# Kernel optimization log

Hardware: AMD Instinct MI355X
Metric: run time of the kernel (lower is better)

Reference implementation:

```python
import jax, jax.numpy as jnp
import numpy as np

def setup_inputs() -> dict:
    key = jax.random.key(0)
    k1, k2 = jax.random.split(key)
    bb_feats = jax.random.normal(k1, (8, 512, 128, 128), dtype=jnp.float32)
    aux_out = jax.random.normal(k2, (8, 19, 128, 128), dtype=jnp.float32)
    return {"bb_feats": bb_feats, "aux_out": aux_out}

def reference(bb_feats, aux_out):
    B, K, H, W = aux_out.shape
    C = bb_feats.shape[1]
    probs = jax.nn.softmax(aux_out.reshape(B, K, H * W), axis=2)  # [B,K,HW]
    feats = bb_feats.reshape(B, C, H * W)                          # [B,C,HW]
    # weighted sum over spatial dim: [B,K,HW] x [B,C,HW] -> [B,K,C]
    ctx = jnp.einsum('bks,bcs->bkc', probs, feats)
    # -> [B,C,K,1]
    return jnp.transpose(ctx, (0, 2, 1))[..., None]
```

## Files before the change

kernel.cpp:

```cpp
#include <hip/hip_runtime.h>
#include <math.h>

#define B 8
#define C 512
#define K 19
#define HW 16384
#define L2E 1.44269504088896340736f

#define CPW 8
#define SCHUNK 4096
#define NSC (HW / SCHUNK)
#define CPB (CPW * 4)
#define CG (C / CPB)

__global__ __launch_bounds__(256)
void softmax_stats_kernel(const float* __restrict__ aux, float* __restrict__ stats) {
    int row = blockIdx.x;
    const float4* x4 = (const float4*)(aux + (size_t)row * HW);
    int tid = threadIdx.x;

    float m = -INFINITY;
    for (int i = tid; i < HW / 4; i += 256) {
        float4 v = x4[i];
        m = fmaxf(m, fmaxf(fmaxf(v.x, v.y), fmaxf(v.z, v.w)));
    }
    #pragma unroll
    for (int off = 32; off > 0; off >>= 1) m = fmaxf(m, __shfl_xor(m, off, 64));
    __shared__ float red[4];
    if ((tid & 63) == 0) red[tid >> 6] = m;
    __syncthreads();
    m = fmaxf(fmaxf(red[0], red[1]), fmaxf(red[2], red[3]));
    __syncthreads();

    float ssum = 0.f;
    for (int i = tid; i < HW / 4; i += 256) {
        float4 v = x4[i];
        ssum += exp2f((v.x - m) * L2E);
        ssum += exp2f((v.y - m) * L2E);
        ssum += exp2f((v.z - m) * L2E);
        ssum += exp2f((v.w - m) * L2E);
    }
    #pragma unroll
    for (int off = 32; off > 0; off >>= 1) ssum += __shfl_xor(ssum, off, 64);
    if ((tid & 63) == 0) red[tid >> 6] = ssum;
    __syncthreads();
    if (tid == 0) {
        float Z = red[0] + red[1] + red[2] + red[3];
        stats[row * 2]     = -m * L2E;
        stats[row * 2 + 1] = 1.0f / Z;
    }
}

__global__ __launch_bounds__(256, 2)
void gather_kernel(const float* __restrict__ feats, const float* __restrict__ aux,
                   const float* __restrict__ stats, float* __restrict__ out) {
    int bid  = blockIdx.x;
    int sc   = bid & (NSC - 1);
    int cg   = (bid / NSC) & (CG - 1);
    int b    = bid / (NSC * CG);
    int lane = threadIdx.x & 63;
    int wave = threadIdx.x >> 6;
    int c0   = cg * CPB + wave * CPW;

    const float* Abase = aux   + (size_t)b * K * HW;
    const float* Fbase = feats + ((size_t)b * C + c0) * HW;
    const float* S     = stats + (size_t)b * K * 2;

    float negml[K], invz[K];
    #pragma unroll
    for (int k = 0; k < K; k++) { negml[k] = S[2 * k]; invz[k] = S[2 * k + 1]; }

    float acc[CPW][K];
    #pragma unroll
    for (int c = 0; c < CPW; c++)
        #pragma unroll
        for (int k = 0; k < K; k++) acc[c][k] = 0.f;

    int s0 = sc * SCHUNK + lane;
    for (int step = 0; step < SCHUNK / 64; step++) {
        int s = s0 + step * 64;
        float p[K];
        #pragma unroll
        for (int k = 0; k < K; k++) {
            float a = Abase[(size_t)k * HW + s];
            p[k] = exp2f(fmaf(a, L2E, negml[k])) * invz[k];
        }
        #pragma unroll
        for (int c = 0; c < CPW; c++) {
            float f = Fbase[(size_t)c * HW + s];
            #pragma unroll
            for (int k = 0; k < K; k++) acc[c][k] = fmaf(p[k], f, acc[c][k]);
        }
    }

    #pragma unroll
    for (int c = 0; c < CPW; c++)
        #pragma unroll
        for (int k = 0; k < K; k++) {
            float v = acc[c][k];
            #pragma unroll
            for (int off = 32; off > 0; off >>= 1) v += __shfl_xor(v, off, 64);
            acc[c][k] = v;
        }

    if (lane == 0) {
        #pragma unroll
        for (int c = 0; c < CPW; c++)
            #pragma unroll
            for (int k = 0; k < K; k++)
                atomicAdd(&out[((size_t)b * C + c0 + c) * K + k], acc[c][k]);
    }
}

extern "C" void kernel_launch(void* const* d_in, const int* in_sizes, int n_in,
                              void* d_out, int out_size, void* d_ws, size_t ws_size,
                              hipStream_t stream) {
    const float* feats = (const float*)d_in[0];
    const float* aux   = (const float*)d_in[1];
    float* out   = (float*)d_out;
    float* stats = (float*)d_ws;

    hipMemsetAsync(d_out, 0, (size_t)out_size * sizeof(float), stream);
    softmax_stats_kernel<<<B * K, 256, 0, stream>>>(aux, stats);
    gather_kernel<<<B * CG * NSC, 256, 0, stream>>>(feats, aux, stats, out);
}
```

Baseline: 482.7 us.

## Share softmax probabilities across waves via LDS and vectorize feature loads

After: 1.368 ms. +183.4%, slower.

```diff
diff --git a/kernel.cpp b/kernel.cpp
--- a/kernel.cpp
+++ b/kernel.cpp
@@ -7,34 +7,42 @@
 #define HW 16384
 #define L2E 1.44269504088896340736f
 
-#define CPW 8
-#define SCHUNK 4096
-#define NSC (HW / SCHUNK)
-#define CPB (CPW * 4)
+#define NW 4
+#define CPW 4
+#define CPB (CPW * NW)
 #define CG (C / CPB)
+#define NSC 4
+#define SCHUNK (HW / NSC)
+#define TS 256
+#define NT (SCHUNK / TS)
 
-__global__ __launch_bounds__(256)
+__global__ __launch_bounds__(1024)
 void softmax_stats_kernel(const float* __restrict__ aux, float* __restrict__ stats) {
     int row = blockIdx.x;
     const float4* x4 = (const float4*)(aux + (size_t)row * HW);
-    int tid = threadIdx.x;
+    int tid  = threadIdx.x;
+    int lane = tid & 63;
+    int wave = tid >> 6;
+    __shared__ float red[16];
 
     float m = -INFINITY;
-    for (int i = tid; i < HW / 4; i += 256) {
-        float4 v = x4[i];
+    #pragma unroll
+    for (int i = 0; i < 4; i++) {
+        float4 v = x4[tid + i * 1024];
         m = fmaxf(m, fmaxf(fmaxf(v.x, v.y), fmaxf(v.z, v.w)));
     }
     #pragma unroll
     for (int off = 32; off > 0; off >>= 1) m = fmaxf(m, __shfl_xor(m, off, 64));
-    __shared__ float red[4];
-    if ((tid & 63) == 0) red[tid >> 6] = m;
+    if (lane == 0) red[wave] = m;
     __syncthreads();
-    m = fmaxf(fmaxf(red[0], red[1]), fmaxf(red[2], red[3]));
+    #pragma unroll
+    for (int w = 0; w < 16; w++) m = fmaxf(m, red[w]);
     __syncthreads();
 
     float ssum = 0.f;
-    for (int i = tid; i < HW / 4; i += 256) {
-        float4 v = x4[i];
+    #pragma unroll
+    for (int i = 0; i < 4; i++) {
+        float4 v = x4[tid + i * 1024];
         ssum += exp2f((v.x - m) * L2E);
         ssum += exp2f((v.y - m) * L2E);
         ssum += exp2f((v.z - m) * L2E);
@@ -42,33 +50,41 @@
     }
     #pragma unroll
     for (int off = 32; off > 0; off >>= 1) ssum += __shfl_xor(ssum, off, 64);
-    if ((tid & 63) == 0) red[tid >> 6] = ssum;
+    if (lane == 0) red[wave] = ssum;
     __syncthreads();
     if (tid == 0) {
-        float Z = red[0] + red[1] + red[2] + red[3];
+        float Z = 0.f;
+        #pragma unroll
+        for (int w = 0; w < 16; w++) Z += red[w];
         stats[row * 2]     = -m * L2E;
         stats[row * 2 + 1] = 1.0f / Z;
     }
 }
 
-__global__ __launch_bounds__(256, 2)
+__global__ __launch_bounds__(256, 4)
 void gather_kernel(const float* __restrict__ feats, const float* __restrict__ aux,
                    const float* __restrict__ stats, float* __restrict__ out) {
+    __shared__ float plds[K][TS];
+
     int bid  = blockIdx.x;
     int sc   = bid & (NSC - 1);
     int cg   = (bid / NSC) & (CG - 1);
     int b    = bid / (NSC * CG);
-    int lane = threadIdx.x & 63;
-    int wave = threadIdx.x >> 6;
+    int tid  = threadIdx.x;
+    int lane = tid & 63;
+    int wave = tid >> 6;
     int c0   = cg * CPB + wave * CPW;
 
-    const float* Abase = aux   + (size_t)b * K * HW;
-    const float* Fbase = feats + ((size_t)b * C + c0) * HW;
+    const float* Abase = aux   + (size_t)b * K * HW + sc * SCHUNK;
+    const float* Fbase = feats + ((size_t)b * C + c0) * HW + sc * SCHUNK;
     const float* S     = stats + (size_t)b * K * 2;
 
     float negml[K], invz[K];
     #pragma unroll
-    for (int k = 0; k < K; k++) { negml[k] = S[2 * k]; invz[k] = S[2 * k + 1]; }
+    for (int k = 0; k < K; k++) {
+        negml[k] = __int_as_float(__builtin_amdgcn_readfirstlane(__float_as_int(S[2 * k])));
+        invz[k]  = __int_as_float(__builtin_amdgcn_readfirstlane(__float_as_int(S[2 * k + 1])));
+    }
 
     float acc[CPW][K];
     #pragma unroll
@@ -76,20 +92,31 @@
         #pragma unroll
         for (int k = 0; k < K; k++) acc[c][k] = 0.f;
 
-    int s0 = sc * SCHUNK + lane;
-    for (int step = 0; step < SCHUNK / 64; step++) {
-        int s = s0 + step * 64;
-        float p[K];
+    for (int t = 0; t < NT; t++) {
+        int s0 = t * TS;
+
+        __syncthreads();
         #pragma unroll
         for (int k = 0; k < K; k++) {
-            float a = Abase[(size_t)k * HW + s];
-            p[k] = exp2f(fmaf(a, L2E, negml[k])) * invz[k];
+            float a = Abase[k * HW + s0 + tid];
+            plds[k][tid] = exp2f(fmaf(a, L2E, negml[k])) * invz[k];
         }
+        __syncthreads();
+
+        float4 f[CPW];
         #pragma unroll
-        for (int c = 0; c < CPW; c++) {
-            float f = Fbase[(size_t)c * HW + s];
+        for (int c = 0; c < CPW; c++)
+            f[c] = *(const float4*)(Fbase + c * HW + s0 + lane * 4);
+        #pragma unroll
+        for (int k = 0; k < K; k++) {
+            float4 p4 = *(const float4*)(&plds[k][lane * 4]);
             #pragma unroll
-            for (int k = 0; k < K; k++) acc[c][k] = fmaf(p[k], f, acc[c][k]);
+            for (int c = 0; c < CPW; c++) {
+                acc[c][k] = fmaf(p4.x, f[c].x, acc[c][k]);
+                acc[c][k] = fmaf(p4.y, f[c].y, acc[c][k]);
+                acc[c][k] = fmaf(p4.z, f[c].z, acc[c][k]);
+                acc[c][k] = fmaf(p4.w, f[c].w, acc[c][k]);
+            }
         }
     }
 
@@ -100,16 +127,9 @@
             float v = acc[c][k];
             #pragma unroll
             for (int off = 32; off > 0; off >>= 1) v += __shfl_xor(v, off, 64);
-            acc[c][k] = v;
+            if (lane == 0)
+                atomicAdd(&out[((size_t)b * C + c0 + c) * K + k], v);
         }
-
-    if (lane == 0) {
-        #pragma unroll
-        for (int c = 0; c < CPW; c++)
-            #pragma unroll
-            for (int k = 0; k < K; k++)
-                atomicAdd(&out[((size_t)b * C + c0 + c) * K + k], acc[c][k]);
-    }
 }
 
 extern "C" void kernel_launch(void* const* d_in, const int* in_sizes, int n_in,
@@ -121,6 +141,6 @@
     float* stats = (float*)d_ws;
 
     hipMemsetAsync(d_out, 0, (size_t)out_size * sizeof(float), stream);
-    softmax_stats_kernel<<<B * K, 256, 0, stream>>>(aux, stats);
+    softmax_stats_kernel<<<B * K, 1024, 0, stream>>>(aux, stats);
     gather_kernel<<<B * CG * NSC, 256, 0, stream>>>(feats, aux, stats, out);
 }
```
